# Kernel optimization log

Hardware: AMD Instinct MI355X
Metric: run time of the kernel (lower is better)

The kernel has to match this reference:

```python
import jax, jax.numpy as jnp
import numpy as np

N_NODES = 100000
N_EDGES = 3200000
D_IN = 128
D_HID = 16
N_CLS = 2


def gcn_conv(x, edge_index, W, b, n_nodes):
    """PyG GCNConv (normalize=True, add_self_loops=True, bias=True)."""
    h = x @ W  # [N, out]
    loop = jnp.arange(n_nodes, dtype=edge_index.dtype)
    src = jnp.concatenate([edge_index[0], loop])
    dst = jnp.concatenate([edge_index[1], loop])
    deg = jax.ops.segment_sum(jnp.ones_like(dst, dtype=h.dtype), dst, num_segments=n_nodes)
    dinv = jnp.where(deg > 0, jax.lax.rsqrt(deg), jnp.zeros_like(deg))
    norm = dinv[src] * dinv[dst]  # [E+N]
    msg = h[src] * norm[:, None]  # gather + scale
    out = jax.ops.segment_sum(msg, dst, num_segments=n_nodes)  # scatter-add
    return out + b


def setup_inputs() -> dict:
    key = jax.random.key(0)
    k1, k2, k3, k4, k5 = jax.random.split(key, 5)
    x = jax.random.normal(k1, (N_NODES, D_IN), dtype=jnp.float32)
    edge_index = jax.random.randint(k2, (2, N_EDGES), 0, N_NODES, dtype=jnp.int64)
    # Glorot-style init for GCNConv weights, zeros for bias (PyG default)
    W1 = jax.random.normal(k3, (D_IN, D_HID), dtype=jnp.float32) * (1.0 / np.sqrt(D_IN))
    b1 = jnp.zeros((D_HID,), dtype=jnp.float32)
    W2 = jax.random.normal(k4, (D_HID, N_CLS), dtype=jnp.float32) * (1.0 / np.sqrt(D_HID))
    b2 = jnp.zeros((N_CLS,), dtype=jnp.float32)
    return {"x": x, "edge_index": edge_index, "W1": W1, "b1": b1, "W2": W2, "b2": b2}


def reference(x, edge_index, W1, b1, W2, b2):
    n = x.shape[0]
    h = gcn_conv(x, edge_index, W1, b1, n)
    h = jax.nn.relu(h)
    # dropout is identity in eval mode
    h = gcn_conv(h, edge_index, W2, b2, n)
    return jax.nn.log_softmax(h, axis=1)
```

## Files before the change

### kernel.cpp

```cpp
#include <hip/hip_runtime.h>
#include <hip/hip_bf16.h>
#include <hip/hip_fp16.h>

#define D_IN  128
#define D_HID 16
#define N_CLS 2
#define NPB   256
#define MAXB  512
#define TILE  4096
#define XROW  136

#define FE 0

typedef short bf16x8 __attribute__((ext_vector_type(8)));
typedef float f32x4  __attribute__((ext_vector_type(4)));

__device__ __forceinline__ unsigned short f2bf(float f) {
    unsigned int u = __float_as_uint(f);
    u += 0x7FFFu + ((u >> 16) & 1u);
    return (unsigned short)(u >> 16);
}

template<bool I64>
__device__ __forceinline__ int lde(const void* p, size_t i) {
    if constexpr (I64) return (int)((const long long*)p)[i];
    else               return ((const int*)p)[i];
}

__global__ void k_detect(const int* __restrict__ ev, int* __restrict__ flags) {
    __shared__ int sE;
    if (threadIdx.x == 0) sE = 0;
    __syncthreads();
    if (ev[2 * threadIdx.x + 1] != 0) atomicOr(&sE, 1);
    __syncthreads();
    if (threadIdx.x == 0) flags[FE] = sE ? 0 : 1;
}

template<bool I64>
__device__ __forceinline__ void part_body(
        const void* __restrict__ ei, unsigned int* __restrict__ gcur,
        unsigned int* __restrict__ staged, int E, int cap,
        unsigned int* sbuf, unsigned short* bbuf,
        int* hist, int* lbase, int* gb, int* wsum) {
    int tid = threadIdx.x;
    int t0 = blockIdx.x * TILE;

    hist[tid] = 0;
    __syncthreads();

    int myB[8]; unsigned int myP[8]; int myR[8];
#pragma unroll
    for (int k = 0; k < 8; ++k) {
        int e = t0 + k * 512 + tid;
        if (e < E) {
            int s = lde<I64>(ei, (size_t)e);
            int d = lde<I64>(ei, (size_t)E + e);
            int b = d >> 8;
            myB[k] = b;
            myP[k] = ((unsigned int)s << 8) | (unsigned int)(d & 255);
            myR[k] = atomicAdd(&hist[b], 1);
        } else myB[k] = -1;
    }
    __syncthreads();

    int v = hist[tid];
    int lane = tid & 63, wv = tid >> 6;
    int s = v;
#pragma unroll
    for (int m = 1; m < 64; m <<= 1) {
        int t = __shfl_up(s, m, 64);
        if (lane >= m) s += t;
    }
    if (lane == 63) wsum[wv] = s;
    __syncthreads();
    int woff = 0;
#pragma unroll
    for (int w = 0; w < 8; ++w) if (w < wv) woff += wsum[w];
    int excl = s + woff - v;
    lbase[tid] = excl;
    int gb_ = 0;
    if (v > 0) gb_ = (int)atomicAdd(&gcur[tid], (unsigned int)v);
    gb[tid] = gb_;
    __syncthreads();

#pragma unroll
    for (int k = 0; k < 8; ++k) {
        if (myB[k] >= 0) {
            int pos = lbase[myB[k]] + myR[k];
            sbuf[pos] = myP[k];
            bbuf[pos] = (unsigned short)myB[k];
        }
    }
    __syncthreads();

    int tot = lbase[MAXB - 1] + hist[MAXB - 1];
    for (int i = tid; i < tot; i += 512) {
        int b = bbuf[i];
        int rel = gb[b] + (i - lbase[b]);
        if (rel < cap)
            staged[(size_t)b * cap + rel] = sbuf[i];
    }
}

__global__ __launch_bounds__(512) void k_part(
        const void* __restrict__ ei, unsigned int* __restrict__ gcur,
        unsigned int* __restrict__ staged, int E, int cap) {
    __shared__ unsigned int sbuf[TILE];
    __shared__ unsigned short bbuf[TILE];
    __shared__ int hist[MAXB], lbase[MAXB], gb[MAXB];
    __shared__ int wsum[8];
    __shared__ int sI64;
    int tid = threadIdx.x;
    if (tid == 0) sI64 = 1;
    __syncthreads();
    if (tid < 256 && 2 * tid + 1 < 2 * E && ((const int*)ei)[2 * tid + 1] != 0) sI64 = 0;
    __syncthreads();
    if (sI64) part_body<true >(ei, gcur, staged, E, cap, sbuf, bbuf, hist, lbase, gb, wsum);
    else      part_body<false>(ei, gcur, staged, E, cap, sbuf, bbuf, hist, lbase, gb, wsum);
}

__global__ __launch_bounds__(512) void k_sortd(
        const unsigned int* __restrict__ staged, const unsigned int* __restrict__ gcur,
        unsigned int* __restrict__ staged2, unsigned int* __restrict__ dmeta,
        float* __restrict__ dinv, int cap, int N) {
    __shared__ unsigned int h[NPB];
    __shared__ unsigned int cur[NPB];
    __shared__ int wsum[4];
    int tid = threadIdx.x, b = blockIdx.x;
    long long s0 = (long long)b * cap;
    int cnt = (int)gcur[b];
    if (cnt > cap) cnt = cap;
    if (tid < NPB) h[tid] = 0u;
    __syncthreads();
    for (int i = tid; i < cnt; i += 512)
        atomicAdd(&h[staged[s0 + i] & 255], 1u);
    __syncthreads();
    int v = 0, sIncl = 0;
    int lane = tid & 63, wv = tid >> 6;
    if (tid < NPB) {
        v = (int)h[tid];
        sIncl = v;
#pragma unroll
        for (int m = 1; m < 64; m <<= 1) {
            int t = __shfl_up(sIncl, m, 64);
            if (lane >= m) sIncl += t;
        }
        if (lane == 63) wsum[wv] = sIncl;
    }
    __syncthreads();
    if (tid < NPB) {
        int woff = 0;
#pragma unroll
        for (int w = 0; w < 4; ++w) if (w < wv) woff += wsum[w];
        int excl = sIncl + woff - v;
        int node = b * NPB + tid;
        dmeta[node] = ((unsigned int)excl << 16) | (unsigned int)v;
        cur[tid] = (unsigned int)excl;
        if (node < N) dinv[node] = rsqrtf((float)(v + 1));
    }
    __syncthreads();
    for (int i = tid; i < cnt; i += 512) {
        unsigned int p = staged[s0 + i];
        unsigned int r = atomicAdd(&cur[p & 255], 1u);
        staged2[s0 + r] = p;
    }
}

__global__ __launch_bounds__(256) void k_gemm1m(
        const float* __restrict__ x, const float* __restrict__ W1,
        const float* __restrict__ dinv, __half* __restrict__ g1h, int n) {
    __shared__ short xhi[64 * XROW];
    __shared__ short xlo[64 * XROW];
    __shared__ short whi[16 * XROW];
    __shared__ short wlo[16 * XROW];
    int tid = threadIdx.x;
    int node0 = blockIdx.x * 64;

    for (int i = tid; i < D_IN * D_HID; i += 256) {
        int k = i >> 4, f = i & 15;
        float v = W1[i];
        unsigned short h = f2bf(v);
        float fh = __uint_as_float(((unsigned int)h) << 16);
        whi[f * XROW + k] = (short)h;
        wlo[f * XROW + k] = (short)f2bf(v - fh);
    }
    int limFlat = (n - node0) * D_IN;
#pragma unroll
    for (int it = 0; it < 8; ++it) {
        int flat = it * 1024 + tid * 4;
        float4 v = make_float4(0.f, 0.f, 0.f, 0.f);
        if (flat < limFlat) v = *(const float4*)(x + (size_t)node0 * D_IN + flat);
        int row = flat >> 7, k = flat & 127;
        unsigned short h0 = f2bf(v.x), h1 = f2bf(v.y), h2 = f2bf(v.z), h3 = f2bf(v.w);
        unsigned short l0 = f2bf(v.x - __uint_as_float(((unsigned int)h0) << 16));
        unsigned short l1 = f2bf(v.y - __uint_as_float(((unsigned int)h1) << 16));
        unsigned short l2 = f2bf(v.z - __uint_as_float(((unsigned int)h2) << 16));
        unsigned short l3 = f2bf(v.w - __uint_as_float(((unsigned int)h3) << 16));
        int o = row * XROW + k;
        *(uint2*)(&xhi[o]) = make_uint2((unsigned int)h0 | ((unsigned int)h1 << 16),
                                        (unsigned int)h2 | ((unsigned int)h3 << 16));
        *(uint2*)(&xlo[o]) = make_uint2((unsigned int)l0 | ((unsigned int)l1 << 16),
                                        (unsigned int)l2 | ((unsigned int)l3 << 16));
    }
    __syncthreads();

    int w = tid >> 6, L = tid & 63;
    int m = L & 15, q = L >> 4;
    const short* axh = &xhi[(w * 16 + m) * XROW + q * 8];
    const short* axl = &xlo[(w * 16 + m) * XROW + q * 8];
    const short* bwh = &whi[m * XROW + q * 8];
    const short* bwl = &wlo[m * XROW + q * 8];
    f32x4 acc = {0.f, 0.f, 0.f, 0.f};
#pragma unroll
    for (int c = 0; c < 4; ++c) {
        bf16x8 ah = *(const bf16x8*)(axh + c * 32);
        bf16x8 al = *(const bf16x8*)(axl + c * 32);
        bf16x8 bh = *(const bf16x8*)(bwh + c * 32);
        bf16x8 bl = *(const bf16x8*)(bwl + c * 32);
        acc = __builtin_amdgcn_mfma_f32_16x16x32_bf16(ah, bh, acc, 0, 0, 0);
        acc = __builtin_amdgcn_mfma_f32_16x16x32_bf16(ah, bl, acc, 0, 0, 0);
        acc = __builtin_amdgcn_mfma_f32_16x16x32_bf16(al, bh, acc, 0, 0, 0);
    }
    int nodeB = node0 + w * 16 + q * 4;
#pragma unroll
    for (int r = 0; r < 4; ++r) {
        int node = nodeB + r;
        if (node < n) g1h[(size_t)node * D_HID + m] = __float2half(dinv[node] * acc[r]);
    }
}

__global__ __launch_bounds__(256) void k_agg1w(
        const unsigned int* __restrict__ staged2, const unsigned int* __restrict__ dmeta,
        const __half* __restrict__ g1h, const float* __restrict__ dinv,
        const float* __restrict__ b1, const float* __restrict__ W2,
        float2* __restrict__ g2, int N, int cap) {
    int tid = threadIdx.x, b = blockIdx.x, by = blockIdx.y;
    long long s0 = (long long)b * cap;
    int lane = tid & 63;
    int f2 = lane & 7;
    int e8 = lane >> 3;
    int wid = (by << 2) + (tid >> 6);
    const __half2* g1h2 = (const __half2*)g1h;
    int f0 = f2 * 2;
    float b10 = b1[f0], b11 = b1[f0 + 1];
    float w00 = W2[f0 * N_CLS + 0], w01 = W2[f0 * N_CLS + 1];
    float w10 = W2[(f0 + 1) * N_CLS + 0], w11 = W2[(f0 + 1) * N_CLS + 1];
    unsigned int md[8];
#pragma unroll
    for (int k = 0; k < 8; ++k) md[k] = dmeta[b * NPB + wid + (k << 5)];
#pragma unroll 2
    for (int k = 0; k < 8; ++k) {
        int dl = wid + (k << 5);
        int node = b * NPB + dl;
        long long st = s0 + (md[k] >> 16);
        int deg = (int)(md[k] & 0xFFFFu);
        float ax = 0.f, ay = 0.f;
        for (int base = 0; base < deg; base += 64) {
            int rem = deg - base;
#pragma unroll
            for (int j = 0; j < 8; ++j) {
                int ei = (j << 3) + e8;
                if (ei < rem) {
                    unsigned int pe = staged2[st + base + ei];
                    float2 t = __half22float2(g1h2[(size_t)(pe >> 8) * 8 + f2]);
                    ax += t.x; ay += t.y;
                }
            }
        }
        ax += __shfl_xor(ax, 8, 64);  ay += __shfl_xor(ay, 8, 64);
        ax += __shfl_xor(ax, 16, 64); ay += __shfl_xor(ay, 16, 64);
        ax += __shfl_xor(ax, 32, 64); ay += __shfl_xor(ay, 32, 64);
        float c0 = 0.f, c1 = 0.f, di = 0.f;
        if (node < N) {
            float2 t = __half22float2(g1h2[(size_t)node * 8 + f2]);
            ax += t.x; ay += t.y;
            di = dinv[node];
            float r0 = fmaxf(b10 + di * ax, 0.f);
            float r1 = fmaxf(b11 + di * ay, 0.f);
            c0 = r0 * w00 + r1 * w10;
            c1 = r0 * w01 + r1 * w11;
        }
        c0 += __shfl_xor(c0, 1, 64); c1 += __shfl_xor(c1, 1, 64);
        c0 += __shfl_xor(c0, 2, 64); c1 += __shfl_xor(c1, 2, 64);
        c0 += __shfl_xor(c0, 4, 64); c1 += __shfl_xor(c1, 4, 64);
        if (lane == 0 && node < N) g2[node] = make_float2(di * c0, di * c1);
    }
}

__global__ __launch_bounds__(256) void k_agg2w(
        const unsigned int* __restrict__ staged2, const unsigned int* __restrict__ dmeta,
        const float2* __restrict__ g2, const float* __restrict__ dinv,
        const float* __restrict__ b2, float2* __restrict__ out, int N, int cap) {
    int tid = threadIdx.x, b = blockIdx.x, by = blockIdx.y;
    long long s0 = (long long)b * cap;
    int lane = tid & 63;
    int wid = (by << 2) + (tid >> 6);
    float bb0 = b2[0], bb1 = b2[1];
    unsigned int md[8];
#pragma unroll
    for (int k = 0; k < 8; ++k) md[k] = dmeta[b * NPB + wid + (k << 5)];
#pragma unroll 2
    for (int k = 0; k < 8; ++k) {
        int dl = wid + (k << 5);
        int node = b * NPB + dl;
        long long st = s0 + (md[k] >> 16);
        int deg = (int)(md[k] & 0xFFFFu);
        float a0 = 0.f, a1 = 0.f;
        for (int base = 0; base < deg; base += 64) {
            int rem = deg - base;
            if (lane < rem) {
                unsigned int p = staged2[st + base + lane];
                float2 t = g2[p >> 8];
                a0 += t.x; a1 += t.y;
            }
        }
#pragma unroll
        for (int mm = 1; mm < 64; mm <<= 1) {
            a0 += __shfl_xor(a0, mm, 64);
            a1 += __shfl_xor(a1, mm, 64);
        }
        if (lane == 0 && node < N) {
            float2 self = g2[node];
            float di = dinv[node];
            float v0 = bb0 + di * (a0 + self.x);
            float v1 = bb1 + di * (a1 + self.y);
            float mx = fmaxf(v0, v1);
            float lse = mx + logf(expf(v0 - mx) + expf(v1 - mx));
            out[node] = make_float2(v0 - lse, v1 - lse);
        }
    }
}

__global__ void fb_deg_init(unsigned int* __restrict__ deg, int n) {
    int i = blockIdx.x * blockDim.x + threadIdx.x;
    if (i < n) deg[i] = 1u;
}
template<bool I64>
__global__ void fb_deg_count(const void* __restrict__ ei, unsigned int* __restrict__ deg,
                             int E, const int* __restrict__ flags) {
    if (flags[FE] != (int)I64) return;
    int e = blockIdx.x * blockDim.x + threadIdx.x;
    if (e < E) atomicAdd(&deg[lde<I64>(ei, (size_t)E + e)], 1u);
}
__global__ void fb_dinv_inplace(float* __restrict__ dinv, int n) {
    int i = blockIdx.x * blockDim.x + threadIdx.x;
    if (i < n) {
        unsigned int u = ((const unsigned int*)dinv)[i];
        dinv[i] = rsqrtf((float)u);
    }
}
__global__ void fb_a1_init(const float* __restrict__ h1, const float* __restrict__ dinv,
                           const float* __restrict__ b1, float* __restrict__ a1, int n) {
    int tid = blockIdx.x * blockDim.x + threadIdx.x;
    if (tid >= n * D_HID) return;
    int node = tid >> 4, f = tid & 15;
    float di = dinv[node];
    a1[tid] = b1[f] + di * di * h1[tid];
}
template<bool I64>
__global__ void fb_agg1(const void* __restrict__ ei, const float* __restrict__ dinv,
                        const float* __restrict__ h1, float* __restrict__ a1,
                        int E, const int* __restrict__ flags) {
    if (flags[FE] != (int)I64) return;
    int tid = blockIdx.x * blockDim.x + threadIdx.x;
    int e = tid >> 4, f = tid & 15;
    if (e >= E) return;
    int s = lde<I64>(ei, (size_t)e);
    int d = lde<I64>(ei, (size_t)E + e);
    float norm = dinv[s] * dinv[d];
    atomicAdd(&a1[(size_t)d * D_HID + f], h1[(size_t)s * D_HID + f] * norm);
}
__global__ void fb_relu_gemm2(const float* __restrict__ a1, const float* __restrict__ W2,
                              float* __restrict__ h2, int n) {
    int node = blockIdx.x * blockDim.x + threadIdx.x;
    if (node >= n) return;
    float c0 = 0.f, c1 = 0.f;
    const float* row = a1 + (size_t)node * D_HID;
#pragma unroll
    for (int f = 0; f < D_HID; ++f) {
        float r = fmaxf(row[f], 0.f);
        c0 += r * W2[f * N_CLS + 0];
        c1 += r * W2[f * N_CLS + 1];
    }
    h2[(size_t)node * 2 + 0] = c0;
    h2[(size_t)node * 2 + 1] = c1;
}
__global__ void fb_a2_init(const float* __restrict__ h2, const float* __restrict__ dinv,
                           const float* __restrict__ b2, float* __restrict__ a2, int n) {
    int tid = blockIdx.x * blockDim.x + threadIdx.x;
    if (tid >= n * N_CLS) return;
    int node = tid >> 1, c = tid & 1;
    float di = dinv[node];
    a2[tid] = b2[c] + di * di * h2[tid];
}
template<bool I64>
__global__ void fb_agg2(const void* __restrict__ ei, const float* __restrict__ dinv,
                        const float* __restrict__ h2, float* __restrict__ a2,
                        int E, const int* __restrict__ flags) {
    if (flags[FE] != (int)I64) return;
    int e = blockIdx.x * blockDim.x + threadIdx.x;
    if (e >= E) return;
    int s = lde<I64>(ei, (size_t)e);
    int d = lde<I64>(ei, (size_t)E + e);
    float norm = dinv[s] * dinv[d];
    atomicAdd(&a2[(size_t)d * 2 + 0], h2[(size_t)s * 2 + 0] * norm);
    atomicAdd(&a2[(size_t)d * 2 + 1], h2[(size_t)s * 2 + 1] * norm);
}
__global__ void fb_gemm1(const float* __restrict__ x, const float* __restrict__ W1,
                         float* __restrict__ h1, int n) {
    __shared__ float w[D_IN * D_HID];
    for (int i = threadIdx.x; i < D_IN * D_HID; i += blockDim.x) w[i] = W1[i];
    __syncthreads();
    int tid = blockIdx.x * blockDim.x + threadIdx.x;
    int node = tid >> 4, f = tid & 15;
    if (node >= n) return;
    const float4* xr = (const float4*)(x + (size_t)node * D_IN);
    float acc = 0.f;
#pragma unroll
    for (int k4 = 0; k4 < D_IN / 4; ++k4) {
        float4 v = xr[k4];
        int k = k4 * 4;
        acc += v.x * w[(k + 0) * D_HID + f];
        acc += v.y * w[(k + 1) * D_HID + f];
        acc += v.z * w[(k + 2) * D_HID + f];
        acc += v.w * w[(k + 3) * D_HID + f];
    }
    h1[tid] = acc;
}
__global__ void fb_lsm(const float* __restrict__ a2, float* __restrict__ out, int n) {
    int node = blockIdx.x * blockDim.x + threadIdx.x;
    if (node >= n) return;
    float v0 = a2[(size_t)node * 2 + 0];
    float v1 = a2[(size_t)node * 2 + 1];
    float m = fmaxf(v0, v1);
    float lse = m + logf(expf(v0 - m) + expf(v1 - m));
    out[(size_t)node * 2 + 0] = v0 - lse;
    out[(size_t)node * 2 + 1] = v1 - lse;
}

extern "C" void kernel_launch(void* const* d_in, const int* in_sizes, int n_in,
                              void* d_out, int out_size, void* d_ws, size_t ws_size,
                              hipStream_t stream) {
    const float* x  = (const float*)d_in[0];
    const void*  ei = d_in[1];
    const float* W1 = (const float*)d_in[2];
    const float* b1 = (const float*)d_in[3];
    const float* W2 = (const float*)d_in[4];
    const float* b2 = (const float*)d_in[5];

    const int N = in_sizes[0] / D_IN;
    const int E = in_sizes[1] / 2;
    const int nb = (N + NPB - 1) / NPB;

    int cap = ((2 * (E / nb + 1)) + 255) & ~255;
    if (cap < 1024) cap = 1024;

    const int B = 256;
    dim3 blk(B);
    const int nBlkN = (N + B - 1) / B;
    const int nBlkE = (E + B - 1) / B;
    char* ws = (char*)d_ws;

    auto al = [](size_t v) { return (v + 255) & ~(size_t)255; };
    const size_t oDinv   = 0;
    const size_t oDmeta  = al(oDinv + (size_t)N * 4);
    const size_t oGcur   = al(oDmeta + (size_t)nb * NPB * 4);
    const size_t oFlag   = al(oGcur + (size_t)MAXB * 4);
    const size_t oStage  = al(oFlag + 8);
    const size_t oStage2 = al(oStage + (size_t)nb * cap * 4);
    const size_t oG1h    = al(oStage2 + (size_t)nb * cap * 4);
    const size_t oG2     = al(oG1h + (size_t)N * D_HID * 2);
    const size_t needNew = al(oG2 + (size_t)N * 2 * 4);

    if (ws_size >= needNew && nb <= MAXB && cap <= 65280 && N < (1 << 24)) {
        float*        dinv    = (float*)(ws + oDinv);
        unsigned int* dmeta   = (unsigned int*)(ws + oDmeta);
        unsigned int* gcur    = (unsigned int*)(ws + oGcur);
        unsigned int* staged  = (unsigned int*)(ws + oStage);
        unsigned int* staged2 = (unsigned int*)(ws + oStage2);
        __half*       g1h     = (__half*)(ws + oG1h);
        float2*       g2      = (float2*)(ws + oG2);

        hipMemsetAsync(gcur, 0, (size_t)nb * 4, stream);

        dim3 gPart((E + TILE - 1) / TILE);
        k_part<<<gPart, dim3(512), 0, stream>>>(ei, gcur, staged, E, cap);

        k_sortd<<<dim3(nb), dim3(512), 0, stream>>>(staged, gcur, staged2, dmeta, dinv, cap, N);

        k_gemm1m<<<dim3((N + 63) / 64), dim3(256), 0, stream>>>(x, W1, dinv, g1h, N);

        k_agg1w<<<dim3(nb, 8), dim3(256), 0, stream>>>(staged2, dmeta, g1h, dinv, b1, W2, g2, N, cap);

        k_agg2w<<<dim3(nb, 8), dim3(256), 0, stream>>>(staged2, dmeta, g2, dinv, b2,
                                                       (float2*)d_out, N, cap);
    } else {
        float* dinv  = (float*)(ws + 0);
        float* h1    = (float*)(ws + 400128);
        float* a1    = (float*)(ws + 6800256);
        float* h2    = (float*)(ws + 13200384);
        float* a2    = (float*)(ws + 14000512);
        int*   flags = (int*)  (ws + 14800640);

        k_detect<<<dim3(1), blk, 0, stream>>>((const int*)ei, flags);
        fb_deg_init<<<dim3(nBlkN), blk, 0, stream>>>((unsigned int*)dinv, N);
        fb_deg_count<false><<<dim3(nBlkE), blk, 0, stream>>>(ei, (unsigned int*)dinv, E, flags);
        fb_deg_count<true ><<<dim3(nBlkE), blk, 0, stream>>>(ei, (unsigned int*)dinv, E, flags);
        fb_dinv_inplace<<<dim3(nBlkN), blk, 0, stream>>>(dinv, N);

        dim3 g_nh((N * D_HID + B - 1) / B);
        fb_gemm1<<<g_nh, blk, 0, stream>>>(x, W1, h1, N);
        fb_a1_init<<<g_nh, blk, 0, stream>>>(h1, dinv, b1, a1, N);
        dim3 g_eh(((size_t)E * D_HID + B - 1) / B);
        fb_agg1<false><<<g_eh, blk, 0, stream>>>(ei, dinv, h1, a1, E, flags);
        fb_agg1<true ><<<g_eh, blk, 0, stream>>>(ei, dinv, h1, a1, E, flags);
        fb_relu_gemm2<<<dim3(nBlkN), blk, 0, stream>>>(a1, W2, h2, N);
        dim3 g_n2((N * N_CLS + B - 1) / B);
        fb_a2_init<<<g_n2, blk, 0, stream>>>(h2, dinv, b2, a2, N);
        fb_agg2<false><<<dim3(nBlkE), blk, 0, stream>>>(ei, dinv, h2, a2, E, flags);
        fb_agg2<true ><<<dim3(nBlkE), blk, 0, stream>>>(ei, dinv, h2, a2, E, flags);
        fb_lsm<<<dim3(nBlkN), blk, 0, stream>>>(a2, (float*)d_out, N);
    }
}
```

Before: 248.0 us.

## Embed self-loops in sorted edge lists and batch index loads before gathers

The sort kernel now reserves one extra slot per destination node and writes a self-loop entry into it. The aggregation kernels can then treat the self term as an ordinary edge and compute dinv from the count instead of loading dinv and the self feature separately. The layer-1 aggregation also loads all eight edge indices into registers before issuing the feature gathers, and both kernels clamp indices in place of branching, so more loads can be in flight at once. In exchange, each staging bucket uses slightly more capacity and the tail lanes do redundant gathers.

Result: faster. 222.1 us (-10.5%).

```diff
diff --git a/kernel.cpp b/kernel.cpp
--- a/kernel.cpp
+++ b/kernel.cpp
@@ -129,7 +129,7 @@
     int tid = threadIdx.x, b = blockIdx.x;
     long long s0 = (long long)b * cap;
     int cnt = (int)gcur[b];
-    if (cnt > cap) cnt = cap;
+    if (cnt > cap - NPB) cnt = cap - NPB;
     if (tid < NPB) h[tid] = 0u;
     __syncthreads();
     for (int i = tid; i < cnt; i += 512)
@@ -154,8 +154,9 @@
         for (int w = 0; w < 4; ++w) if (w < wv) woff += wsum[w];
         int excl = sIncl + woff - v;
         int node = b * NPB + tid;
-        dmeta[node] = ((unsigned int)excl << 16) | (unsigned int)v;
-        cur[tid] = (unsigned int)excl;
+        int start = excl + tid;
+        dmeta[node] = ((unsigned int)start << 16) | (unsigned int)v;
+        cur[tid] = (unsigned int)start;
         if (node < N) dinv[node] = rsqrtf((float)(v + 1));
     }
     __syncthreads();
@@ -163,6 +164,13 @@
         unsigned int p = staged[s0 + i];
         unsigned int r = atomicAdd(&cur[p & 255], 1u);
         staged2[s0 + r] = p;
+    }
+    __syncthreads();
+    if (tid < NPB) {
+        unsigned int pos = cur[tid];
+        int node = b * NPB + tid;
+        if ((int)pos < cap)
+            staged2[s0 + pos] = ((unsigned int)node << 8) | (unsigned int)tid;
     }
 }
 
@@ -231,7 +239,7 @@
 
 __global__ __launch_bounds__(256) void k_agg1w(
         const unsigned int* __restrict__ staged2, const unsigned int* __restrict__ dmeta,
-        const __half* __restrict__ g1h, const float* __restrict__ dinv,
+        const __half* __restrict__ g1h,
         const float* __restrict__ b1, const float* __restrict__ W2,
         float2* __restrict__ g2, int N, int cap) {
     int tid = threadIdx.x, b = blockIdx.x, by = blockIdx.y;
@@ -250,36 +258,33 @@
     for (int k = 0; k < 8; ++k) md[k] = dmeta[b * NPB + wid + (k << 5)];
 #pragma unroll 2
     for (int k = 0; k < 8; ++k) {
-        int dl = wid + (k << 5);
-        int node = b * NPB + dl;
-        long long st = s0 + (md[k] >> 16);
-        int deg = (int)(md[k] & 0xFFFFu);
+        int node = b * NPB + wid + (k << 5);
+        const unsigned int* sp = staged2 + s0 + (md[k] >> 16);
+        int cnt = (int)(md[k] & 0xFFFFu) + 1;
         float ax = 0.f, ay = 0.f;
-        for (int base = 0; base < deg; base += 64) {
-            int rem = deg - base;
+        for (int base = 0; base < cnt; base += 64) {
+            unsigned int pe[8];
 #pragma unroll
             for (int j = 0; j < 8; ++j) {
-                int ei = (j << 3) + e8;
-                if (ei < rem) {
-                    unsigned int pe = staged2[st + base + ei];
-                    float2 t = __half22float2(g1h2[(size_t)(pe >> 8) * 8 + f2]);
-                    ax += t.x; ay += t.y;
-                }
+                int idx = base + (j << 3) + e8;
+                int c = idx < cnt ? idx : cnt - 1;
+                pe[j] = sp[c];
+            }
+#pragma unroll
+            for (int j = 0; j < 8; ++j) {
+                int idx = base + (j << 3) + e8;
+                float2 t = __half22float2(g1h2[(size_t)(pe[j] >> 8) * 8 + f2]);
+                if (idx < cnt) { ax += t.x; ay += t.y; }
             }
         }
         ax += __shfl_xor(ax, 8, 64);  ay += __shfl_xor(ay, 8, 64);
         ax += __shfl_xor(ax, 16, 64); ay += __shfl_xor(ay, 16, 64);
         ax += __shfl_xor(ax, 32, 64); ay += __shfl_xor(ay, 32, 64);
-        float c0 = 0.f, c1 = 0.f, di = 0.f;
-        if (node < N) {
-            float2 t = __half22float2(g1h2[(size_t)node * 8 + f2]);
-            ax += t.x; ay += t.y;
-            di = dinv[node];
-            float r0 = fmaxf(b10 + di * ax, 0.f);
-            float r1 = fmaxf(b11 + di * ay, 0.f);
-            c0 = r0 * w00 + r1 * w10;
-            c1 = r0 * w01 + r1 * w11;
-        }
+        float di = rsqrtf((float)cnt);
+        float r0 = fmaxf(b10 + di * ax, 0.f);
+        float r1 = fmaxf(b11 + di * ay, 0.f);
+        float c0 = r0 * w00 + r1 * w10;
+        float c1 = r0 * w01 + r1 * w11;
         c0 += __shfl_xor(c0, 1, 64); c1 += __shfl_xor(c1, 1, 64);
         c0 += __shfl_xor(c0, 2, 64); c1 += __shfl_xor(c1, 2, 64);
         c0 += __shfl_xor(c0, 4, 64); c1 += __shfl_xor(c1, 4, 64);
@@ -289,7 +294,7 @@
 
 __global__ __launch_bounds__(256) void k_agg2w(
         const unsigned int* __restrict__ staged2, const unsigned int* __restrict__ dmeta,
-        const float2* __restrict__ g2, const float* __restrict__ dinv,
+        const float2* __restrict__ g2,
         const float* __restrict__ b2, float2* __restrict__ out, int N, int cap) {
     int tid = threadIdx.x, b = blockIdx.x, by = blockIdx.y;
     long long s0 = (long long)b * cap;
@@ -301,18 +306,16 @@
     for (int k = 0; k < 8; ++k) md[k] = dmeta[b * NPB + wid + (k << 5)];
 #pragma unroll 2
     for (int k = 0; k < 8; ++k) {
-        int dl = wid + (k << 5);
-        int node = b * NPB + dl;
-        long long st = s0 + (md[k] >> 16);
-        int deg = (int)(md[k] & 0xFFFFu);
+        int node = b * NPB + wid + (k << 5);
+        const unsigned int* sp = staged2 + s0 + (md[k] >> 16);
+        int cnt = (int)(md[k] & 0xFFFFu) + 1;
         float a0 = 0.f, a1 = 0.f;
-        for (int base = 0; base < deg; base += 64) {
-            int rem = deg - base;
-            if (lane < rem) {
-                unsigned int p = staged2[st + base + lane];
-                float2 t = g2[p >> 8];
-                a0 += t.x; a1 += t.y;
-            }
+        for (int base = 0; base < cnt; base += 64) {
+            int idx = base + lane;
+            int c = idx < cnt ? idx : cnt - 1;
+            unsigned int p = sp[c];
+            float2 t = g2[p >> 8];
+            if (idx < cnt) { a0 += t.x; a1 += t.y; }
         }
 #pragma unroll
         for (int mm = 1; mm < 64; mm <<= 1) {
@@ -320,10 +323,9 @@
             a1 += __shfl_xor(a1, mm, 64);
         }
         if (lane == 0 && node < N) {
-            float2 self = g2[node];
-            float di = dinv[node];
-            float v0 = bb0 + di * (a0 + self.x);
-            float v1 = bb1 + di * (a1 + self.y);
+            float di = rsqrtf((float)cnt);
+            float v0 = bb0 + di * a0;
+            float v1 = bb1 + di * a1;
             float mx = fmaxf(v0, v1);
             float lse = mx + logf(expf(v0 - mx) + expf(v1 - mx));
             out[node] = make_float2(v0 - lse, v1 - lse);
@@ -452,7 +454,7 @@
     const int E = in_sizes[1] / 2;
     const int nb = (N + NPB - 1) / NPB;
 
-    int cap = ((2 * (E / nb + 1)) + 255) & ~255;
+    int cap = ((2 * (E / nb + 1) + NPB) + 255) & ~255;
     if (cap < 1024) cap = 1024;
 
     const int B = 256;
@@ -472,7 +474,7 @@
     const size_t oG2     = al(oG1h + (size_t)N * D_HID * 2);
     const size_t needNew = al(oG2 + (size_t)N * 2 * 4);
 
-    if (ws_size >= needNew && nb <= MAXB && cap <= 65280 && N < (1 << 24)) {
+    if (ws_size >= needNew && nb <= MAXB && cap <= 65280 && N < (1 << 24) - NPB) {
         float*        dinv    = (float*)(ws + oDinv);
         unsigned int* dmeta   = (unsigned int*)(ws + oDmeta);
         unsigned int* gcur    = (unsigned int*)(ws + oGcur);
@@ -490,9 +492,9 @@
 
         k_gemm1m<<<dim3((N + 63) / 64), dim3(256), 0, stream>>>(x, W1, dinv, g1h, N);
 
-        k_agg1w<<<dim3(nb, 8), dim3(256), 0, stream>>>(staged2, dmeta, g1h, dinv, b1, W2, g2, N, cap);
-
-        k_agg2w<<<dim3(nb, 8), dim3(256), 0, stream>>>(staged2, dmeta, g2, dinv, b2,
+        k_agg1w<<<dim3(nb, 8), dim3(256), 0, stream>>>(staged2, dmeta, g1h, b1, W2, g2, N, cap);
+
+        k_agg2w<<<dim3(nb, 8), dim3(256), 0, stream>>>(staged2, dmeta, g2, b2,
                                                        (float2*)d_out, N, cap);
     } else {
         float* dinv  = (float*)(ws + 0);
```
